# Optimization experiments

Hardware: AMD Instinct MI355X
Metric: run time of the kernel (lower is better)

The kernel has to match this reference:

```python
import jax, jax.numpy as jnp
import numpy as np

GAMMA = 0.99
LAM = 0.95
CLIP = 0.2
VALUE_COEFF = 0.5
ENTROPY_COEFF = 0.01
T = 500_000
S = 128
A = 16


def _mlp(x, W1, b1, W2, b2, W3, b3):
    h = jax.nn.relu(x @ W1 + b1)
    h = jax.nn.relu(h @ W2 + b2)
    return h @ W3 + b3


def setup_inputs() -> dict:
    key = jax.random.key(0)
    ks = jax.random.split(key, 12)
    states = jax.random.normal(ks[0], (T, S), dtype=jnp.float32)
    next_states = jax.random.normal(ks[1], (T, S), dtype=jnp.float32)
    rewards = jax.random.normal(ks[2], (T,), dtype=jnp.float32)
    dones = (jax.random.uniform(ks[3], (T,)) < 0.01).astype(jnp.float32)
    actions = jax.random.randint(ks[4], (T,), 0, A)
    # old log-probs of taken actions (valid log-probabilities)
    old_logp = jnp.log(jax.random.uniform(ks[5], (T,), minval=1e-3, maxval=1.0))

    def lin(k, fan_in, fan_out):
        lim = 1.0 / np.sqrt(fan_in)
        return jax.random.uniform(k, (fan_in, fan_out), minval=-lim, maxval=lim, dtype=jnp.float32)

    return {
        'states': states, 'next_states': next_states, 'rewards': rewards,
        'dones': dones, 'actions': actions, 'old_logp': old_logp,
        'aW1': lin(ks[6], S, 64), 'ab1': jnp.zeros((64,), jnp.float32),
        'aW2': lin(ks[7], 64, 64), 'ab2': jnp.zeros((64,), jnp.float32),
        'aW3': lin(ks[8], 64, A), 'ab3': jnp.zeros((A,), jnp.float32),
        'cW1': lin(ks[9], S, 64), 'cb1': jnp.zeros((64,), jnp.float32),
        'cW2': lin(ks[10], 64, 64), 'cb2': jnp.zeros((64,), jnp.float32),
        'cW3': lin(ks[11], 64, 1), 'cb3': jnp.zeros((1,), jnp.float32),
    }


def reference(states, next_states, rewards, dones, actions, old_logp,
              aW1, ab1, aW2, ab2, aW3, ab3,
              cW1, cb1, cW2, cb2, cW3, cb3):
    # ---- critic values and TD deltas ----
    values = _mlp(states, cW1, cb1, cW2, cb2, cW3, cb3)[:, 0]        # [T]
    next_values = _mlp(next_states, cW1, cb1, cW2, cb2, cW3, cb3)[:, 0]
    not_done = 1.0 - dones
    deltas = rewards + GAMMA * next_values * not_done - values       # [T]

    # ---- GAE: reverse-time linear recurrence a_t = c_t * a_{t+1} + d_t ----
    coef = GAMMA * LAM * not_done

    def step(carry, cd):
        c, d = cd
        a = c * carry + d
        return a, a

    _, advantages = jax.lax.scan(step, jnp.float32(0.0), (coef, deltas), reverse=True)
    returns = advantages + values
    adv_n = (advantages - advantages.mean()) / (jnp.std(advantages, ddof=1) + 1e-8)

    # ---- actor: clipped surrogate ----
    probs = jax.nn.softmax(_mlp(states, aW1, ab1, aW2, ab2, aW3, ab3), axis=-1)  # [T, A]
    logp = jnp.log(jnp.take_along_axis(probs, actions[:, None], axis=1))[:, 0]   # [T]
    ratios = jnp.exp(logp - old_logp)
    surr1 = ratios * adv_n
    surr2 = jnp.clip(ratios, 1.0 - CLIP, 1.0 + CLIP) * adv_n
    actor_loss = -jnp.minimum(surr1, surr2).mean()

    # ---- critic MSE loss ----
    critic_loss = jnp.mean((values - returns) ** 2)

    # ---- entropy bonus ----
    entropy_loss = jnp.mean(-jnp.sum(probs * jnp.log(probs + 1e-8), axis=-1))

    total_loss = actor_loss + VALUE_COEFF * critic_loss - ENTROPY_COEFF * entropy_loss
    return jnp.stack([total_loss, actor_loss, critic_loss, entropy_loss])
```

## Files before the change

kernel.cpp:

```cpp
#include <hip/hip_runtime.h>
#include <hip/hip_bf16.h>

#define T_N 500000
#define NTILE 31250
#define NBLK 768
#define NWAVES (NBLK * 4)
#define NCHUNK 4096
#define CHUNKL 128
#define NPART 1024

typedef __attribute__((ext_vector_type(8))) short short8v;
typedef __attribute__((ext_vector_type(4))) float float4v;

__device__ __forceinline__ short f2bf(float f) {
    __hip_bfloat16 b = __float2bfloat16(f);
    return *reinterpret_cast<short*>(&b);
}
__device__ __forceinline__ float bf2f(short s) {
    return __uint_as_float(((unsigned)(unsigned short)s) << 16);
}

__device__ __forceinline__ short8v cvt8(const float4 a, const float4 b) {
    short8v r;
    r[0] = f2bf(a.x); r[1] = f2bf(a.y); r[2] = f2bf(a.z); r[3] = f2bf(a.w);
    r[4] = f2bf(b.x); r[5] = f2bf(b.y); r[6] = f2bf(b.z); r[7] = f2bf(b.w);
    return r;
}

#define FC1 0
#define FA1 16
#define FC2 32
#define FA2 40
#define FA3 48
#define NFRAG 50

__device__ __forceinline__ int featperm(int c, int r) {
    return ((c >> 1) << 5) + ((r >> 2) << 3) + ((c & 1) << 2) + (r & 3);
}

__global__ __launch_bounds__(64) void k_pack(
    const float* __restrict__ cW1, const float* __restrict__ aW1,
    const float* __restrict__ cW2, const float* __restrict__ aW2,
    const float* __restrict__ aW3, short8v* __restrict__ packed)
{
    const int f = blockIdx.x, l = threadIdx.x;
    const int g = l >> 4, r = l & 15;
    const float* W; int s, c, ncol; bool perm = true;
    if (f < FA1)      { W = cW1; s = f >> 2;         c = f & 3;         ncol = 64; }
    else if (f < FC2) { W = aW1; s = (f - FA1) >> 2; c = (f - FA1) & 3; ncol = 64; }
    else if (f < FA2) { W = cW2; s = (f - FC2) >> 2; c = (f - FC2) & 3; ncol = 64; }
    else if (f < FA3) { W = aW2; s = (f - FA2) >> 2; c = (f - FA2) & 3; ncol = 64; }
    else              { W = aW3; s = f - FA3;        c = 0;             ncol = 16; perm = false; }
    const int col = perm ? featperm(c, r) : r;
    short8v frag;
    #pragma unroll
    for (int j = 0; j < 8; ++j) {
        int k = s * 32 + g * 8 + j;
        frag[j] = f2bf(W[k * ncol + col]);
    }
    packed[f * 64 + l] = frag;
}

__device__ __forceinline__ void mk_bfrag(const float4v* acc, short8v* bf) {
    #pragma unroll
    for (int s = 0; s < 2; ++s)
        #pragma unroll
        for (int j = 0; j < 8; ++j)
            bf[s][j] = f2bf(fmaxf(acc[2 * s + (j >> 2)][j & 3], 0.f));
}

__global__ __launch_bounds__(256) void k_mlp(
    const float* __restrict__ states, const float* __restrict__ next_states,
    const short8v* __restrict__ pk,
    const float* __restrict__ cb1, const float* __restrict__ ab1,
    const float* __restrict__ cb2, const float* __restrict__ ab2,
    const float* __restrict__ ab3,
    const float* __restrict__ cW3, const float* __restrict__ cb3,
    float* __restrict__ v_o, float* __restrict__ nv_o,
    short* __restrict__ logit_o)
{
    const int l = threadIdx.x & 63;
    const int g = l >> 4, q = l & 15;
    const int wid = blockIdx.x * 4 + (threadIdx.x >> 6);
    const float cb3v = cb3[0];
    int off[4];
    #pragma unroll
    for (int c = 0; c < 4; ++c) off[c] = ((c >> 1) << 5) + (g << 3) + ((c & 1) << 2);

    for (long long t = wid; t < NTILE; t += NWAVES) {
        const long long r0 = t * 16;

        const float* xs = states + (r0 + q) * 128 + g * 8;
        const float* xn = next_states + (r0 + q) * 128 + g * 8;
        float4 ra[8], rb[8];
        #pragma unroll
        for (int s = 0; s < 4; ++s) {
            ra[2 * s]     = *reinterpret_cast<const float4*>(xs + s * 32);
            ra[2 * s + 1] = *reinterpret_cast<const float4*>(xs + s * 32 + 4);
            rb[2 * s]     = *reinterpret_cast<const float4*>(xn + s * 32);
            rb[2 * s + 1] = *reinterpret_cast<const float4*>(xn + s * 32 + 4);
        }
        short8v sa[4], na[4];
        #pragma unroll
        for (int s = 0; s < 4; ++s) {
            sa[s] = cvt8(ra[2 * s], ra[2 * s + 1]);
            na[s] = cvt8(rb[2 * s], rb[2 * s + 1]);
        }

        float4v accC[4], accN[4];
        #pragma unroll
        for (int c = 0; c < 4; ++c) {
            float4 b = *reinterpret_cast<const float4*>(cb1 + off[c]);
            accC[c] = (float4v){b.x, b.y, b.z, b.w};
            accN[c] = accC[c];
        }
        #pragma unroll
        for (int s = 0; s < 4; ++s)
            #pragma unroll
            for (int c = 0; c < 4; ++c) {
                short8v w = pk[(FC1 + s * 4 + c) * 64 + l];
                accC[c] = __builtin_amdgcn_mfma_f32_16x16x32_bf16(w, sa[s], accC[c], 0, 0, 0);
                accN[c] = __builtin_amdgcn_mfma_f32_16x16x32_bf16(w, na[s], accN[c], 0, 0, 0);
            }
        short8v bC[2], bN[2];
        mk_bfrag(accC, bC);
        mk_bfrag(accN, bN);

        float4v c2C[4], c2N[4];
        #pragma unroll
        for (int c = 0; c < 4; ++c) {
            float4 b = *reinterpret_cast<const float4*>(cb2 + off[c]);
            c2C[c] = (float4v){b.x, b.y, b.z, b.w};
            c2N[c] = c2C[c];
        }
        #pragma unroll
        for (int s = 0; s < 2; ++s)
            #pragma unroll
            for (int c = 0; c < 4; ++c) {
                short8v w = pk[(FC2 + s * 4 + c) * 64 + l];
                c2C[c] = __builtin_amdgcn_mfma_f32_16x16x32_bf16(w, bC[s], c2C[c], 0, 0, 0);
                c2N[c] = __builtin_amdgcn_mfma_f32_16x16x32_bf16(w, bN[s], c2N[c], 0, 0, 0);
            }

        float vp = 0.f, np = 0.f;
        #pragma unroll
        for (int c = 0; c < 4; ++c) {
            float4 w3v = *reinterpret_cast<const float4*>(cW3 + off[c]);
            const float wv4[4] = {w3v.x, w3v.y, w3v.z, w3v.w};
            #pragma unroll
            for (int u = 0; u < 4; ++u) {
                vp = fmaf(fmaxf(c2C[c][u], 0.f), wv4[u], vp);
                np = fmaf(fmaxf(c2N[c][u], 0.f), wv4[u], np);
            }
        }
        vp += __shfl_xor(vp, 16); vp += __shfl_xor(vp, 32);
        np += __shfl_xor(np, 16); np += __shfl_xor(np, 32);
        if (g == 0) {
            v_o[r0 + q]  = vp + cb3v;
            nv_o[r0 + q] = np + cb3v;
        }

        float4v aA[4];
        #pragma unroll
        for (int c = 0; c < 4; ++c) {
            float4 b = *reinterpret_cast<const float4*>(ab1 + off[c]);
            aA[c] = (float4v){b.x, b.y, b.z, b.w};
        }
        #pragma unroll
        for (int s = 0; s < 4; ++s)
            #pragma unroll
            for (int c = 0; c < 4; ++c)
                aA[c] = __builtin_amdgcn_mfma_f32_16x16x32_bf16(
                    pk[(FA1 + s * 4 + c) * 64 + l], sa[s], aA[c], 0, 0, 0);
        short8v bA[2];
        mk_bfrag(aA, bA);

        float4v a2[4];
        #pragma unroll
        for (int c = 0; c < 4; ++c) {
            float4 b = *reinterpret_cast<const float4*>(ab2 + off[c]);
            a2[c] = (float4v){b.x, b.y, b.z, b.w};
        }
        #pragma unroll
        for (int s = 0; s < 2; ++s)
            #pragma unroll
            for (int c = 0; c < 4; ++c)
                a2[c] = __builtin_amdgcn_mfma_f32_16x16x32_bf16(
                    pk[(FA2 + s * 4 + c) * 64 + l], bA[s], a2[c], 0, 0, 0);
        short8v b3[2];
        mk_bfrag(a2, b3);

        float4 ab3v = *reinterpret_cast<const float4*>(ab3 + g * 4);
        float4v a3 = (float4v){ab3v.x, ab3v.y, ab3v.z, ab3v.w};
        #pragma unroll
        for (int s = 0; s < 2; ++s)
            a3 = __builtin_amdgcn_mfma_f32_16x16x32_bf16(
                pk[(FA3 + s) * 64 + l], b3[s], a3, 0, 0, 0);

        unsigned w0 = ((unsigned)(unsigned short)f2bf(a3[1]) << 16) |
                      (unsigned)(unsigned short)f2bf(a3[0]);
        unsigned w1 = ((unsigned)(unsigned short)f2bf(a3[3]) << 16) |
                      (unsigned)(unsigned short)f2bf(a3[2]);
        uint2 lw; lw.x = w0; lw.y = w1;
        *reinterpret_cast<uint2*>(logit_o + (r0 + q) * 16 + g * 4) = lw;
    }
}

__device__ __forceinline__ void dc_elem(float v, float nv, float rw, float dn,
                                        float& d, float& c) {
    float nd = 1.f - dn;
    d = fmaf(0.99f * nd, nv, rw) - v;
    c = (0.99f * 0.95f) * nd;
}

__global__ __launch_bounds__(256) void k_gae_chunk(
    const float* __restrict__ v_i, const float* __restrict__ nv_i,
    const float* __restrict__ rewards, const float* __restrict__ dones,
    float* __restrict__ P, float* __restrict__ Q)
{
    const int c = blockIdx.x * 256 + threadIdx.x;
    const long long lo = (long long)c * CHUNKL;
    float p = 1.f, a = 0.f;
    if (lo < T_N) {
        const int n = (int)((T_N - lo < CHUNKL) ? (T_N - lo) : CHUNKL);
        for (int j = (n >> 2) - 1; j >= 0; --j) {
            float4 vv = *reinterpret_cast<const float4*>(&v_i[lo + 4 * j]);
            float4 nn = *reinterpret_cast<const float4*>(&nv_i[lo + 4 * j]);
            float4 rw = *reinterpret_cast<const float4*>(&rewards[lo + 4 * j]);
            float4 dn = *reinterpret_cast<const float4*>(&dones[lo + 4 * j]);
            float d0, c0, d1, c1, d2, c2, d3, c3;
            dc_elem(vv.x, nn.x, rw.x, dn.x, d0, c0);
            dc_elem(vv.y, nn.y, rw.y, dn.y, d1, c1);
            dc_elem(vv.z, nn.z, rw.z, dn.z, d2, c2);
            dc_elem(vv.w, nn.w, rw.w, dn.w, d3, c3);
            a = fmaf(c3, a, d3);
            a = fmaf(c2, a, d2);
            a = fmaf(c1, a, d1);
            a = fmaf(c0, a, d0);
            p *= c0 * c1 * c2 * c3;
        }
    }
    P[c] = p; Q[c] = a;
}

__global__ __launch_bounds__(1024) void k_gae_scan(
    const float* __restrict__ P, const float* __restrict__ Q,
    float* __restrict__ carry)
{
    __shared__ float sp[1024], sq[1024];
    const int t = threadIdx.x, b = t * 4;
    float p = P[b + 3], q = Q[b + 3];
    #pragma unroll
    for (int c = 2; c >= 0; --c) {
        float pc = P[b + c], qc = Q[b + c];
        q = fmaf(pc, q, qc);
        p = pc * p;
    }
    sp[t] = p; sq[t] = q;
    __syncthreads();
    for (int d = 1; d < 1024; d <<= 1) {
        float pp = sp[t], qq = sq[t];
        float p2 = 1.f, q2 = 0.f;
        const bool has = (t + d) < 1024;
        if (has) { p2 = sp[t + d]; q2 = sq[t + d]; }
        __syncthreads();
        if (has) { sp[t] = pp * p2; sq[t] = fmaf(pp, q2, qq); }
        __syncthreads();
    }
    float x = (t + 1 < 1024) ? sq[t + 1] : 0.f;
    #pragma unroll
    for (int c = 3; c >= 0; --c) {
        carry[b + c] = x;
        x = fmaf(P[b + c], x, Q[b + c]);
    }
}

__global__ __launch_bounds__(256) void k_gae_apply(
    const float* __restrict__ v_i, const float* __restrict__ nv_i,
    const float* __restrict__ rewards, const float* __restrict__ dones,
    const float* __restrict__ carry, float* __restrict__ adv,
    float* __restrict__ part)
{
    const int c = blockIdx.x * 256 + threadIdx.x;
    const long long lo = (long long)c * CHUNKL;
    float s = 0.f, s2 = 0.f;
    if (lo < T_N) {
        const int n = (int)((T_N - lo < CHUNKL) ? (T_N - lo) : CHUNKL);
        float a = carry[c];
        for (int j = (n >> 2) - 1; j >= 0; --j) {
            float4 vv = *reinterpret_cast<const float4*>(&v_i[lo + 4 * j]);
            float4 nn = *reinterpret_cast<const float4*>(&nv_i[lo + 4 * j]);
            float4 rw = *reinterpret_cast<const float4*>(&rewards[lo + 4 * j]);
            float4 dn = *reinterpret_cast<const float4*>(&dones[lo + 4 * j]);
            float d0, c0, d1, c1, d2, c2, d3, c3;
            dc_elem(vv.x, nn.x, rw.x, dn.x, d0, c0);
            dc_elem(vv.y, nn.y, rw.y, dn.y, d1, c1);
            dc_elem(vv.z, nn.z, rw.z, dn.z, d2, c2);
            dc_elem(vv.w, nn.w, rw.w, dn.w, d3, c3);
            float a3 = fmaf(c3, a, d3);
            float a2v = fmaf(c2, a3, d2);
            float a1 = fmaf(c1, a2v, d1);
            float a0 = fmaf(c0, a1, d0);
            float4 o; o.x = a0; o.y = a1; o.z = a2v; o.w = a3;
            *reinterpret_cast<float4*>(&adv[lo + 4 * j]) = o;
            a = a0;
            s += a0 + a1 + a2v + a3;
            s2 += a0 * a0 + a1 * a1 + a2v * a2v + a3 * a3;
        }
    }
    #pragma unroll
    for (int o = 32; o > 0; o >>= 1) { s += __shfl_down(s, o); s2 += __shfl_down(s2, o); }
    __shared__ float l0[4], l1[4];
    const int wv = threadIdx.x >> 6, ln = threadIdx.x & 63;
    if (ln == 0) { l0[wv] = s; l1[wv] = s2; }
    __syncthreads();
    if (threadIdx.x == 0) {
        part[blockIdx.x * 2]     = l0[0] + l0[1] + l0[2] + l0[3];
        part[blockIdx.x * 2 + 1] = l1[0] + l1[1] + l1[2] + l1[3];
    }
}

__global__ __launch_bounds__(256) void k_actor(
    const float* __restrict__ adv, const short* __restrict__ logits,
    const float* __restrict__ old_logp, const int* __restrict__ actions,
    const float* __restrict__ part, float* __restrict__ part4)
{
    __shared__ float st[2];
    if (threadIdx.x == 0) {
        float S = 0.f, S2 = 0.f;
        #pragma unroll
        for (int i = 0; i < 16; ++i) { S += part[2 * i]; S2 += part[2 * i + 1]; }
        const float Tf = (float)T_N;
        float mean = S / Tf;
        float var = (S2 - S * S / Tf) / (Tf - 1.f);
        st[0] = mean;
        st[1] = 1.f / (sqrtf(fmaxf(var, 0.f)) + 1e-8f);
    }
    __syncthreads();
    const float mean = st[0], isd = st[1];
    float sm = 0.f, sent = 0.f;
    for (long long i = (long long)blockIdx.x * 256 + threadIdx.x; i < T_N;
         i += (long long)gridDim.x * 256) {
        const short8v* lp = reinterpret_cast<const short8v*>(logits) + i * 2;
        short8v lo0 = lp[0], lo1 = lp[1];
        float lg[16];
        #pragma unroll
        for (int j = 0; j < 8; ++j) { lg[j] = bf2f(lo0[j]); lg[8 + j] = bf2f(lo1[j]); }
        float m = lg[0];
        #pragma unroll
        for (int a = 1; a < 16; ++a) m = fmaxf(m, lg[a]);
        float se = 0.f, tt = 0.f;
        #pragma unroll
        for (int a = 0; a < 16; ++a) {
            float e = __expf(lg[a] - m);
            se += e;
            tt = fmaf(e, lg[a], tt);
        }
        float ls = __logf(se);
        float ent = m + ls - tt / se;
        const int act = actions[i];
        float lsel = lg[0];
        #pragma unroll
        for (int a = 1; a < 16; ++a) lsel = (a == act) ? lg[a] : lsel;
        float logp = lsel - m - ls;
        float rt = __expf(logp - old_logp[i]);
        float an = (adv[i] - mean) * isd;
        sm += fminf(rt * an, fminf(fmaxf(rt, 0.8f), 1.2f) * an);
        sent += ent;
    }
    #pragma unroll
    for (int o = 32; o > 0; o >>= 1) { sm += __shfl_down(sm, o); sent += __shfl_down(sent, o); }
    __shared__ float l0[4], l1[4];
    const int wv = threadIdx.x >> 6, ln = threadIdx.x & 63;
    if (ln == 0) { l0[wv] = sm; l1[wv] = sent; }
    __syncthreads();
    if (threadIdx.x == 0) {
        part4[blockIdx.x * 2]     = l0[0] + l0[1] + l0[2] + l0[3];
        part4[blockIdx.x * 2 + 1] = l1[0] + l1[1] + l1[2] + l1[3];
    }
}

__global__ __launch_bounds__(1024) void k_final(
    const float* __restrict__ part4, const float* __restrict__ part,
    float* __restrict__ out)
{
    const int t = threadIdx.x;
    float sm = part4[t * 2], se = part4[t * 2 + 1];
    #pragma unroll
    for (int o = 32; o > 0; o >>= 1) { sm += __shfl_down(sm, o); se += __shfl_down(se, o); }
    __shared__ float l0[16], l1[16];
    const int wv = t >> 6, ln = t & 63;
    if (ln == 0) { l0[wv] = sm; l1[wv] = se; }
    __syncthreads();
    if (t == 0) {
        float SM = 0.f, SE = 0.f;
        #pragma unroll
        for (int i = 0; i < 16; ++i) { SM += l0[i]; SE += l1[i]; }
        float S2 = 0.f;
        #pragma unroll
        for (int i = 0; i < 16; ++i) S2 += part[2 * i + 1];
        const float Tf = (float)T_N;
        float actor_loss = -SM / Tf;
        float ent_loss = SE / Tf;
        float critic_loss = S2 / Tf;
        float total = actor_loss + 0.5f * critic_loss - 0.01f * ent_loss;
        out[0] = total; out[1] = actor_loss; out[2] = critic_loss; out[3] = ent_loss;
    }
}

extern "C" void kernel_launch(void* const* d_in, const int* in_sizes, int n_in,
                              void* d_out, int out_size, void* d_ws, size_t ws_size,
                              hipStream_t stream) {
    (void)in_sizes; (void)n_in; (void)out_size; (void)ws_size;
    const float* states      = (const float*)d_in[0];
    const float* next_states = (const float*)d_in[1];
    const float* rewards     = (const float*)d_in[2];
    const float* dones       = (const float*)d_in[3];
    const int*   actions     = (const int*)d_in[4];
    const float* old_logp    = (const float*)d_in[5];
    const float* aW1 = (const float*)d_in[6];  const float* ab1 = (const float*)d_in[7];
    const float* aW2 = (const float*)d_in[8];  const float* ab2 = (const float*)d_in[9];
    const float* aW3 = (const float*)d_in[10]; const float* ab3 = (const float*)d_in[11];
    const float* cW1 = (const float*)d_in[12]; const float* cb1 = (const float*)d_in[13];
    const float* cW2 = (const float*)d_in[14]; const float* cb2 = (const float*)d_in[15];
    const float* cW3 = (const float*)d_in[16]; const float* cb3 = (const float*)d_in[17];
    float* out = (float*)d_out;

    short* logits = (short*)d_ws;
    float* fbase = (float*)(logits + (size_t)T_N * 16);
    float* v_ws  = fbase;
    float* nv_ws = fbase + (size_t)T_N;
    float* adv   = fbase + 2 * (size_t)T_N;
    float* P     = fbase + 3 * (size_t)T_N;
    float* Q     = P + NCHUNK;
    float* carry = Q + NCHUNK;
    float* part  = carry + NCHUNK;
    float* part4 = part + 32;
    short8v* packed = (short8v*)(part4 + 2048);

    k_pack<<<NFRAG, 64, 0, stream>>>(cW1, aW1, cW2, aW2, aW3, packed);
    k_mlp<<<NBLK, 256, 0, stream>>>(
        states, next_states, packed,
        cb1, ab1, cb2, ab2, ab3, cW3, cb3, v_ws, nv_ws, logits);
    k_gae_chunk<<<NCHUNK / 256, 256, 0, stream>>>(v_ws, nv_ws, rewards, dones, P, Q);
    k_gae_scan<<<1, 1024, 0, stream>>>(P, Q, carry);
    k_gae_apply<<<NCHUNK / 256, 256, 0, stream>>>(v_ws, nv_ws, rewards, dones, carry, adv, part);
    k_actor<<<NPART, 256, 0, stream>>>(adv, logits, old_logp, actions, part, part4);
    k_final<<<1, 1024, 0, stream>>>(part4, part, out);
}
```

Baseline: 207.9 us.

## Keep MLP weights in registers and prefetch next tile's inputs in k_mlp

Restructures the MLP kernel into single-wave blocks, 1024 in total. Each wave loads all packed weight fragments and biases into registers once, instead of re-reading them from global memory on every tile. It also software-pipelines the loop: the next tile's states and next_states are loaded while the current tile's MFMAs run, hiding load latency. The cost is much higher register pressure, which can reduce occupancy or cause spills, and fewer total waves (1024 instead of 3072) to hide latency.

```diff
diff --git a/kernel.cpp b/kernel.cpp
--- a/kernel.cpp
+++ b/kernel.cpp
@@ -3,8 +3,8 @@
 
 #define T_N 500000
 #define NTILE 31250
-#define NBLK 768
-#define NWAVES (NBLK * 4)
+#define NBLK 1024
+#define NWAVES NBLK
 #define NCHUNK 4096
 #define CHUNKL 128
 #define NPART 1024
@@ -69,7 +69,7 @@
             bf[s][j] = f2bf(fmaxf(acc[2 * s + (j >> 2)][j & 3], 0.f));
 }
 
-__global__ __launch_bounds__(256) void k_mlp(
+__global__ __launch_bounds__(64) void k_mlp(
     const float* __restrict__ states, const float* __restrict__ next_states,
     const short8v* __restrict__ pk,
     const float* __restrict__ cb1, const float* __restrict__ ab1,
@@ -79,20 +79,33 @@
     float* __restrict__ v_o, float* __restrict__ nv_o,
     short* __restrict__ logit_o)
 {
-    const int l = threadIdx.x & 63;
+    const int l = threadIdx.x;
     const int g = l >> 4, q = l & 15;
-    const int wid = blockIdx.x * 4 + (threadIdx.x >> 6);
+    const int wid = blockIdx.x;
     const float cb3v = cb3[0];
     int off[4];
     #pragma unroll
     for (int c = 0; c < 4; ++c) off[c] = ((c >> 1) << 5) + (g << 3) + ((c & 1) << 2);
 
-    for (long long t = wid; t < NTILE; t += NWAVES) {
-        const long long r0 = t * 16;
-
-        const float* xs = states + (r0 + q) * 128 + g * 8;
-        const float* xn = next_states + (r0 + q) * 128 + g * 8;
-        float4 ra[8], rb[8];
+    short8v wf[NFRAG];
+    #pragma unroll
+    for (int f = 0; f < NFRAG; ++f) wf[f] = pk[f * 64 + l];
+
+    float4 bc1v[4], bc2v[4], ba1v[4], ba2v[4], w3v[4];
+    #pragma unroll
+    for (int c = 0; c < 4; ++c) {
+        bc1v[c] = *reinterpret_cast<const float4*>(cb1 + off[c]);
+        bc2v[c] = *reinterpret_cast<const float4*>(cb2 + off[c]);
+        ba1v[c] = *reinterpret_cast<const float4*>(ab1 + off[c]);
+        ba2v[c] = *reinterpret_cast<const float4*>(ab2 + off[c]);
+        w3v[c]  = *reinterpret_cast<const float4*>(cW3 + off[c]);
+    }
+    float4 ab3v = *reinterpret_cast<const float4*>(ab3 + g * 4);
+
+    float4 ra[8], rb[8];
+    {
+        const float* xs = states + ((long long)wid * 16 + q) * 128 + g * 8;
+        const float* xn = next_states + ((long long)wid * 16 + q) * 128 + g * 8;
         #pragma unroll
         for (int s = 0; s < 4; ++s) {
             ra[2 * s]     = *reinterpret_cast<const float4*>(xs + s * 32);
@@ -100,6 +113,11 @@
             rb[2 * s]     = *reinterpret_cast<const float4*>(xn + s * 32);
             rb[2 * s + 1] = *reinterpret_cast<const float4*>(xn + s * 32 + 4);
         }
+    }
+
+    for (long long t = wid; t < NTILE; t += NWAVES) {
+        const long long r0 = t * 16;
+
         short8v sa[4], na[4];
         #pragma unroll
         for (int s = 0; s < 4; ++s) {
@@ -107,20 +125,30 @@
             na[s] = cvt8(rb[2 * s], rb[2 * s + 1]);
         }
 
+        if (t + NWAVES < NTILE) {
+            const float* xs = states + ((t + NWAVES) * 16 + q) * 128 + g * 8;
+            const float* xn = next_states + ((t + NWAVES) * 16 + q) * 128 + g * 8;
+            #pragma unroll
+            for (int s = 0; s < 4; ++s) {
+                ra[2 * s]     = *reinterpret_cast<const float4*>(xs + s * 32);
+                ra[2 * s + 1] = *reinterpret_cast<const float4*>(xs + s * 32 + 4);
+                rb[2 * s]     = *reinterpret_cast<const float4*>(xn + s * 32);
+                rb[2 * s + 1] = *reinterpret_cast<const float4*>(xn + s * 32 + 4);
+            }
+        }
+
         float4v accC[4], accN[4];
         #pragma unroll
         for (int c = 0; c < 4; ++c) {
-            float4 b = *reinterpret_cast<const float4*>(cb1 + off[c]);
-            accC[c] = (float4v){b.x, b.y, b.z, b.w};
+            accC[c] = (float4v){bc1v[c].x, bc1v[c].y, bc1v[c].z, bc1v[c].w};
             accN[c] = accC[c];
         }
         #pragma unroll
         for (int s = 0; s < 4; ++s)
             #pragma unroll
             for (int c = 0; c < 4; ++c) {
-                short8v w = pk[(FC1 + s * 4 + c) * 64 + l];
-                accC[c] = __builtin_amdgcn_mfma_f32_16x16x32_bf16(w, sa[s], accC[c], 0, 0, 0);
-                accN[c] = __builtin_amdgcn_mfma_f32_16x16x32_bf16(w, na[s], accN[c], 0, 0, 0);
+                accC[c] = __builtin_amdgcn_mfma_f32_16x16x32_bf16(wf[FC1 + s * 4 + c], sa[s], accC[c], 0, 0, 0);
+                accN[c] = __builtin_amdgcn_mfma_f32_16x16x32_bf16(wf[FC1 + s * 4 + c], na[s], accN[c], 0, 0, 0);
             }
         short8v bC[2], bN[2];
         mk_bfrag(accC, bC);
@@ -129,24 +157,21 @@
         float4v c2C[4], c2N[4];
         #pragma unroll
         for (int c = 0; c < 4; ++c) {
-            float4 b = *reinterpret_cast<const float4*>(cb2 + off[c]);
-            c2C[c] = (float4v){b.x, b.y, b.z, b.w};
+            c2C[c] = (float4v){bc2v[c].x, bc2v[c].y, bc2v[c].z, bc2v[c].w};
             c2N[c] = c2C[c];
         }
         #pragma unroll
         for (int s = 0; s < 2; ++s)
             #pragma unroll
             for (int c = 0; c < 4; ++c) {
-                short8v w = pk[(FC2 + s * 4 + c) * 64 + l];
-                c2C[c] = __builtin_amdgcn_mfma_f32_16x16x32_bf16(w, bC[s], c2C[c], 0, 0, 0);
-                c2N[c] = __builtin_amdgcn_mfma_f32_16x16x32_bf16(w, bN[s], c2N[c], 0, 0, 0);
+                c2C[c] = __builtin_amdgcn_mfma_f32_16x16x32_bf16(wf[FC2 + s * 4 + c], bC[s], c2C[c], 0, 0, 0);
+                c2N[c] = __builtin_amdgcn_mfma_f32_16x16x32_bf16(wf[FC2 + s * 4 + c], bN[s], c2N[c], 0, 0, 0);
             }
 
         float vp = 0.f, np = 0.f;
         #pragma unroll
         for (int c = 0; c < 4; ++c) {
-            float4 w3v = *reinterpret_cast<const float4*>(cW3 + off[c]);
-            const float wv4[4] = {w3v.x, w3v.y, w3v.z, w3v.w};
+            const float wv4[4] = {w3v[c].x, w3v[c].y, w3v[c].z, w3v[c].w};
             #pragma unroll
             for (int u = 0; u < 4; ++u) {
                 vp = fmaf(fmaxf(c2C[c][u], 0.f), wv4[u], vp);
@@ -162,40 +187,32 @@
 
         float4v aA[4];
         #pragma unroll
-        for (int c = 0; c < 4; ++c) {
-            float4 b = *reinterpret_cast<const float4*>(ab1 + off[c]);
-            aA[c] = (float4v){b.x, b.y, b.z, b.w};
-        }
+        for (int c = 0; c < 4; ++c)
+            aA[c] = (float4v){ba1v[c].x, ba1v[c].y, ba1v[c].z, ba1v[c].w};
         #pragma unroll
         for (int s = 0; s < 4; ++s)
             #pragma unroll
             for (int c = 0; c < 4; ++c)
-                aA[c] = __builtin_amdgcn_mfma_f32_16x16x32_bf16(
-                    pk[(FA1 + s * 4 + c) * 64 + l], sa[s], aA[c], 0, 0, 0);
+                aA[c] = __builtin_amdgcn_mfma_f32_16x16x32_bf16(wf[FA1 + s * 4 + c], sa[s], aA[c], 0, 0, 0);
         short8v bA[2];
         mk_bfrag(aA, bA);
 
         float4v a2[4];
         #pragma unroll
-        for (int c = 0; c < 4; ++c) {
-            float4 b = *reinterpret_cast<const float4*>(ab2 + off[c]);
-            a2[c] = (float4v){b.x, b.y, b.z, b.w};
-        }
+        for (int c = 0; c < 4; ++c)
+            a2[c] = (float4v){ba2v[c].x, ba2v[c].y, ba2v[c].z, ba2v[c].w};
         #pragma unroll
         for (int s = 0; s < 2; ++s)
             #pragma unroll
             for (int c = 0; c < 4; ++c)
-                a2[c] = __builtin_amdgcn_mfma_f32_16x16x32_bf16(
-                    pk[(FA2 + s * 4 + c) * 64 + l], bA[s], a2[c], 0, 0, 0);
+                a2[c] = __builtin_amdgcn_mfma_f32_16x16x32_bf16(wf[FA2 + s * 4 + c], bA[s], a2[c], 0, 0, 0);
         short8v b3[2];
         mk_bfrag(a2, b3);
 
-        float4 ab3v = *reinterpret_cast<const float4*>(ab3 + g * 4);
         float4v a3 = (float4v){ab3v.x, ab3v.y, ab3v.z, ab3v.w};
         #pragma unroll
         for (int s = 0; s < 2; ++s)
-            a3 = __builtin_amdgcn_mfma_f32_16x16x32_bf16(
-                pk[(FA3 + s) * 64 + l], b3[s], a3, 0, 0, 0);
+            a3 = __builtin_amdgcn_mfma_f32_16x16x32_bf16(wf[FA3 + s], b3[s], a3, 0, 0, 0);
 
         unsigned w0 = ((unsigned)(unsigned short)f2bf(a3[1]) << 16) |
                       (unsigned)(unsigned short)f2bf(a3[0]);
@@ -439,7 +456,7 @@
     short8v* packed = (short8v*)(part4 + 2048);
 
     k_pack<<<NFRAG, 64, 0, stream>>>(cW1, aW1, cW2, aW2, aW3, packed);
-    k_mlp<<<NBLK, 256, 0, stream>>>(
+    k_mlp<<<NBLK, 64, 0, stream>>>(
         states, next_states, packed,
         cb1, ab1, cb2, ab2, ab3, cW3, cb3, v_ws, nv_ws, logits);
     k_gae_chunk<<<NCHUNK / 256, 256, 0, stream>>>(v_ws, nv_ws, rewards, dones, P, Q);
```

Measured after the change: 193.2 us. 7.1% less time.

## Serialize critic/actor passes in MLP kernel to cut registers and raise occupancy

Applied to the files above, without the earlier changes.

Restructures the MLP kernel so the states and next_states passes run one after the other with a single shared accumulator set, instead of interleaving both critic passes. The next_states loads move to after the actor pass. The kernel also gets a min-4-blocks launch bound, and the grid grows from 768 to 1024 blocks. The aim is lower VGPR pressure and more waves in flight to hide memory latency. In exchange, MFMA chains from the two inputs no longer interleave, and each tile has a serial second load phase.

```diff
diff --git a/kernel.cpp b/kernel.cpp
--- a/kernel.cpp
+++ b/kernel.cpp
@@ -3,7 +3,7 @@
 
 #define T_N 500000
 #define NTILE 31250
-#define NBLK 768
+#define NBLK 1024
 #define NWAVES (NBLK * 4)
 #define NCHUNK 4096
 #define CHUNKL 128
@@ -69,7 +69,7 @@
             bf[s][j] = f2bf(fmaxf(acc[2 * s + (j >> 2)][j & 3], 0.f));
 }
 
-__global__ __launch_bounds__(256) void k_mlp(
+__global__ __launch_bounds__(256, 4) void k_mlp(
     const float* __restrict__ states, const float* __restrict__ next_states,
     const short8v* __restrict__ pk,
     const float* __restrict__ cb1, const float* __restrict__ ab1,
@@ -90,119 +90,144 @@
     for (long long t = wid; t < NTILE; t += NWAVES) {
         const long long r0 = t * 16;
 
-        const float* xs = states + (r0 + q) * 128 + g * 8;
-        const float* xn = next_states + (r0 + q) * 128 + g * 8;
-        float4 ra[8], rb[8];
-        #pragma unroll
-        for (int s = 0; s < 4; ++s) {
-            ra[2 * s]     = *reinterpret_cast<const float4*>(xs + s * 32);
-            ra[2 * s + 1] = *reinterpret_cast<const float4*>(xs + s * 32 + 4);
-            rb[2 * s]     = *reinterpret_cast<const float4*>(xn + s * 32);
-            rb[2 * s + 1] = *reinterpret_cast<const float4*>(xn + s * 32 + 4);
-        }
-        short8v sa[4], na[4];
-        #pragma unroll
-        for (int s = 0; s < 4; ++s) {
-            sa[s] = cvt8(ra[2 * s], ra[2 * s + 1]);
-            na[s] = cvt8(rb[2 * s], rb[2 * s + 1]);
-        }
-
-        float4v accC[4], accN[4];
+        short8v sa[4];
+        {
+            const float* xs = states + (r0 + q) * 128 + g * 8;
+            #pragma unroll
+            for (int s = 0; s < 4; ++s) {
+                float4 a = *reinterpret_cast<const float4*>(xs + s * 32);
+                float4 b = *reinterpret_cast<const float4*>(xs + s * 32 + 4);
+                sa[s] = cvt8(a, b);
+            }
+        }
+        float4v acc[4];
+        short8v bf[2];
+
         #pragma unroll
         for (int c = 0; c < 4; ++c) {
             float4 b = *reinterpret_cast<const float4*>(cb1 + off[c]);
-            accC[c] = (float4v){b.x, b.y, b.z, b.w};
-            accN[c] = accC[c];
+            acc[c] = (float4v){b.x, b.y, b.z, b.w};
         }
         #pragma unroll
         for (int s = 0; s < 4; ++s)
             #pragma unroll
+            for (int c = 0; c < 4; ++c)
+                acc[c] = __builtin_amdgcn_mfma_f32_16x16x32_bf16(
+                    pk[(FC1 + s * 4 + c) * 64 + l], sa[s], acc[c], 0, 0, 0);
+        mk_bfrag(acc, bf);
+
+        #pragma unroll
+        for (int c = 0; c < 4; ++c) {
+            float4 b = *reinterpret_cast<const float4*>(cb2 + off[c]);
+            acc[c] = (float4v){b.x, b.y, b.z, b.w};
+        }
+        #pragma unroll
+        for (int s = 0; s < 2; ++s)
+            #pragma unroll
+            for (int c = 0; c < 4; ++c)
+                acc[c] = __builtin_amdgcn_mfma_f32_16x16x32_bf16(
+                    pk[(FC2 + s * 4 + c) * 64 + l], bf[s], acc[c], 0, 0, 0);
+
+        {
+            float vp = 0.f;
+            #pragma unroll
             for (int c = 0; c < 4; ++c) {
-                short8v w = pk[(FC1 + s * 4 + c) * 64 + l];
-                accC[c] = __builtin_amdgcn_mfma_f32_16x16x32_bf16(w, sa[s], accC[c], 0, 0, 0);
-                accN[c] = __builtin_amdgcn_mfma_f32_16x16x32_bf16(w, na[s], accN[c], 0, 0, 0);
+                float4 w3v = *reinterpret_cast<const float4*>(cW3 + off[c]);
+                const float w4[4] = {w3v.x, w3v.y, w3v.z, w3v.w};
+                #pragma unroll
+                for (int u = 0; u < 4; ++u)
+                    vp = fmaf(fmaxf(acc[c][u], 0.f), w4[u], vp);
             }
-        short8v bC[2], bN[2];
-        mk_bfrag(accC, bC);
-        mk_bfrag(accN, bN);
-
-        float4v c2C[4], c2N[4];
+            vp += __shfl_xor(vp, 16); vp += __shfl_xor(vp, 32);
+            if (g == 0) v_o[r0 + q] = vp + cb3v;
+        }
+
+        #pragma unroll
+        for (int c = 0; c < 4; ++c) {
+            float4 b = *reinterpret_cast<const float4*>(ab1 + off[c]);
+            acc[c] = (float4v){b.x, b.y, b.z, b.w};
+        }
+        #pragma unroll
+        for (int s = 0; s < 4; ++s)
+            #pragma unroll
+            for (int c = 0; c < 4; ++c)
+                acc[c] = __builtin_amdgcn_mfma_f32_16x16x32_bf16(
+                    pk[(FA1 + s * 4 + c) * 64 + l], sa[s], acc[c], 0, 0, 0);
+        mk_bfrag(acc, bf);
+
+        #pragma unroll
+        for (int c = 0; c < 4; ++c) {
+            float4 b = *reinterpret_cast<const float4*>(ab2 + off[c]);
+            acc[c] = (float4v){b.x, b.y, b.z, b.w};
+        }
+        #pragma unroll
+        for (int s = 0; s < 2; ++s)
+            #pragma unroll
+            for (int c = 0; c < 4; ++c)
+                acc[c] = __builtin_amdgcn_mfma_f32_16x16x32_bf16(
+                    pk[(FA2 + s * 4 + c) * 64 + l], bf[s], acc[c], 0, 0, 0);
+        mk_bfrag(acc, bf);
+
+        {
+            float4 b3 = *reinterpret_cast<const float4*>(ab3 + g * 4);
+            float4v a3 = (float4v){b3.x, b3.y, b3.z, b3.w};
+            #pragma unroll
+            for (int s = 0; s < 2; ++s)
+                a3 = __builtin_amdgcn_mfma_f32_16x16x32_bf16(
+                    pk[(FA3 + s) * 64 + l], bf[s], a3, 0, 0, 0);
+            unsigned w0 = ((unsigned)(unsigned short)f2bf(a3[1]) << 16) |
+                          (unsigned)(unsigned short)f2bf(a3[0]);
+            unsigned w1 = ((unsigned)(unsigned short)f2bf(a3[3]) << 16) |
+                          (unsigned)(unsigned short)f2bf(a3[2]);
+            uint2 lw; lw.x = w0; lw.y = w1;
+            *reinterpret_cast<uint2*>(logit_o + (r0 + q) * 16 + g * 4) = lw;
+        }
+
+        {
+            const float* xn = next_states + (r0 + q) * 128 + g * 8;
+            #pragma unroll
+            for (int s = 0; s < 4; ++s) {
+                float4 a = *reinterpret_cast<const float4*>(xn + s * 32);
+                float4 b = *reinterpret_cast<const float4*>(xn + s * 32 + 4);
+                sa[s] = cvt8(a, b);
+            }
+        }
+        #pragma unroll
+        for (int c = 0; c < 4; ++c) {
+            float4 b = *reinterpret_cast<const float4*>(cb1 + off[c]);
+            acc[c] = (float4v){b.x, b.y, b.z, b.w};
+        }
+        #pragma unroll
+        for (int s = 0; s < 4; ++s)
+            #pragma unroll
+            for (int c = 0; c < 4; ++c)
+                acc[c] = __builtin_amdgcn_mfma_f32_16x16x32_bf16(
+                    pk[(FC1 + s * 4 + c) * 64 + l], sa[s], acc[c], 0, 0, 0);
+        mk_bfrag(acc, bf);
         #pragma unroll
         for (int c = 0; c < 4; ++c) {
             float4 b = *reinterpret_cast<const float4*>(cb2 + off[c]);
-            c2C[c] = (float4v){b.x, b.y, b.z, b.w};
-            c2N[c] = c2C[c];
+            acc[c] = (float4v){b.x, b.y, b.z, b.w};
         }
         #pragma unroll
         for (int s = 0; s < 2; ++s)
             #pragma unroll
+            for (int c = 0; c < 4; ++c)
+                acc[c] = __builtin_amdgcn_mfma_f32_16x16x32_bf16(
+                    pk[(FC2 + s * 4 + c) * 64 + l], bf[s], acc[c], 0, 0, 0);
+        {
+            float np = 0.f;
+            #pragma unroll
             for (int c = 0; c < 4; ++c) {
-                short8v w = pk[(FC2 + s * 4 + c) * 64 + l];
-                c2C[c] = __builtin_amdgcn_mfma_f32_16x16x32_bf16(w, bC[s], c2C[c], 0, 0, 0);
-                c2N[c] = __builtin_amdgcn_mfma_f32_16x16x32_bf16(w, bN[s], c2N[c], 0, 0, 0);
+                float4 w3v = *reinterpret_cast<const float4*>(cW3 + off[c]);
+                const float w4[4] = {w3v.x, w3v.y, w3v.z, w3v.w};
+                #pragma unroll
+                for (int u = 0; u < 4; ++u)
+                    np = fmaf(fmaxf(acc[c][u], 0.f), w4[u], np);
             }
-
-        float vp = 0.f, np = 0.f;
-        #pragma unroll
-        for (int c = 0; c < 4; ++c) {
-            float4 w3v = *reinterpret_cast<const float4*>(cW3 + off[c]);
-            const float wv4[4] = {w3v.x, w3v.y, w3v.z, w3v.w};
-            #pragma unroll
-            for (int u = 0; u < 4; ++u) {
-                vp = fmaf(fmaxf(c2C[c][u], 0.f), wv4[u], vp);
-                np = fmaf(fmaxf(c2N[c][u], 0.f), wv4[u], np);
-            }
-        }
-        vp += __shfl_xor(vp, 16); vp += __shfl_xor(vp, 32);
-        np += __shfl_xor(np, 16); np += __shfl_xor(np, 32);
-        if (g == 0) {
-            v_o[r0 + q]  = vp + cb3v;
-            nv_o[r0 + q] = np + cb3v;
-        }
-
-        float4v aA[4];
-        #pragma unroll
-        for (int c = 0; c < 4; ++c) {
-            float4 b = *reinterpret_cast<const float4*>(ab1 + off[c]);
-            aA[c] = (float4v){b.x, b.y, b.z, b.w};
-        }
-        #pragma unroll
-        for (int s = 0; s < 4; ++s)
-            #pragma unroll
-            for (int c = 0; c < 4; ++c)
-                aA[c] = __builtin_amdgcn_mfma_f32_16x16x32_bf16(
-                    pk[(FA1 + s * 4 + c) * 64 + l], sa[s], aA[c], 0, 0, 0);
-        short8v bA[2];
-        mk_bfrag(aA, bA);
-
-        float4v a2[4];
-        #pragma unroll
-        for (int c = 0; c < 4; ++c) {
-            float4 b = *reinterpret_cast<const float4*>(ab2 + off[c]);
-            a2[c] = (float4v){b.x, b.y, b.z, b.w};
-        }
-        #pragma unroll
-        for (int s = 0; s < 2; ++s)
-            #pragma unroll
-            for (int c = 0; c < 4; ++c)
-                a2[c] = __builtin_amdgcn_mfma_f32_16x16x32_bf16(
-                    pk[(FA2 + s * 4 + c) * 64 + l], bA[s], a2[c], 0, 0, 0);
-        short8v b3[2];
-        mk_bfrag(a2, b3);
-
-        float4 ab3v = *reinterpret_cast<const float4*>(ab3 + g * 4);
-        float4v a3 = (float4v){ab3v.x, ab3v.y, ab3v.z, ab3v.w};
-        #pragma unroll
-        for (int s = 0; s < 2; ++s)
-            a3 = __builtin_amdgcn_mfma_f32_16x16x32_bf16(
-                pk[(FA3 + s) * 64 + l], b3[s], a3, 0, 0, 0);
-
-        unsigned w0 = ((unsigned)(unsigned short)f2bf(a3[1]) << 16) |
-                      (unsigned)(unsigned short)f2bf(a3[0]);
-        unsigned w1 = ((unsigned)(unsigned short)f2bf(a3[3]) << 16) |
-                      (unsigned)(unsigned short)f2bf(a3[2]);
-        uint2 lw; lw.x = w0; lw.y = w1;
-        *reinterpret_cast<uint2*>(logit_o + (r0 + q) * 16 + g * 4) = lw;
+            np += __shfl_xor(np, 16); np += __shfl_xor(np, 32);
+            if (g == 0) nv_o[r0 + q] = np + cb3v;
+        }
     }
 }
 
```

New measurement: 564.9 us. 172% more time.
